# Optimization experiments

Measured on AMD Instinct MI355X. Metric: run time of the kernel, lower is better.

The kernel has to match this reference:

```python
import jax, jax.numpy as jnp
import numpy as np

TEMP = 0.05          # self.temp
NUM_LABELED = 15080  # SysuDataset bank size


def setup_inputs() -> dict:
    key = jax.random.key(0)
    k1, k2, k3, k4, k5 = jax.random.split(key, 5)
    B, D, L = 512, 2048, NUM_LABELED
    f = jax.random.normal(k1, (B, D), jnp.float32)
    features = f / jnp.linalg.norm(f, axis=1, keepdims=True)  # L2-normalized embeddings
    fk = jax.random.normal(k2, (B, D), jnp.float32)
    features_k = fk / jnp.linalg.norm(fk, axis=1, keepdims=True)
    gt_labels = jax.random.randint(k3, (B, 5), 0, L)   # last column = pid index
    gt_labels_k = jax.random.randint(k4, (B, 5), 0, L)
    bank = jax.random.normal(k5, (L, D), jnp.float32)
    bank_features = bank / jnp.linalg.norm(bank, axis=1, keepdims=True)
    return {"features": features, "features_k": features_k,
            "gt_labels": gt_labels, "gt_labels_k": gt_labels_k,
            "bank_features": bank_features}


def reference(features, features_k, gt_labels, gt_labels_k, bank_features):
    # pids = cat([i[:, -1] for i in gt_labels]); all >= 0 by construction, so the
    # pids > -1 filter is an identity (static shapes under jit).
    pids = gt_labels[:, -1]                                  # [B]
    # HM.forward: inputs.mm(features.t()), then /= temp
    sim_all = (features @ bank_features.T) / TEMP            # [B, L]
    # segment-mean of logits grouped by memory label (labels == arange -> identity,
    # kept for faithfulness to the index_add / nums normalization in the source)
    labels = jnp.arange(NUM_LABELED)
    sim = jax.ops.segment_sum(sim_all.T, labels, num_segments=NUM_LABELED)  # [L, B]
    nums = jax.ops.segment_sum(jnp.ones((NUM_LABELED, 1), jnp.float32),
                               labels, num_segments=NUM_LABELED)            # [L, 1]
    sim = sim / nums
    logits = sim.T                                           # [B, L]
    logp = jax.nn.log_softmax(logits, axis=-1)
    loss = -jnp.mean(jnp.take_along_axis(logp, pids[:, None], axis=1))
    return loss
```

## Files before the change

kernel.cpp:

```cpp
#include <hip/hip_runtime.h>
#include <hip/hip_bf16.h>

#define M_ROWS 512
#define N_COLS 15080
#define K_DIM  2048
#define BM 128
#define BN 128
#define BKF 64
#define NT 118
#define KSTEPS (K_DIM / BKF)
#define SCALE 20.0f

typedef _Float16 f16x8 __attribute__((ext_vector_type(8)));
typedef float    f32x4 __attribute__((ext_vector_type(4)));

extern "C" __global__ __launch_bounds__(256, 2)
void k_gemm_lse(const float* __restrict__ A,
                const float* __restrict__ Bk,
                const int*   __restrict__ gt,
                float* __restrict__ pm,
                float* __restrict__ ps,
                float* __restrict__ tv)
{
    __shared__ __align__(16) ushort lds[16384];

    const int t  = threadIdx.x;
    const int bx = blockIdx.x;

    int mi, nt;
    if (bx < 448) {
        const int slot = bx & 7;
        const int rest = bx >> 3;
        mi = rest & 3;
        nt = (rest >> 2) * 8 + slot;
    } else {
        const int r2 = bx - 448;
        mi = r2 & 3;
        nt = 112 + (r2 >> 2);
    }
    const int rowA0 = mi * BM;
    const int rowB0 = nt * BN;

    int arow[4], ag[4];
#pragma unroll
    for (int i = 0; i < 4; i++) { int G = t + i * 256; arow[i] = G >> 3; ag[i] = G & 7; }

    float4 ra[8], rb[8];
    auto LOAD = [&](int kt) {
#pragma unroll
        for (int i = 0; i < 4; i++) {
            const float* pa = A + (size_t)(rowA0 + arow[i]) * K_DIM + kt * BKF + ag[i] * 8;
            ra[2 * i]     = *(const float4*)(pa);
            ra[2 * i + 1] = *(const float4*)(pa + 4);
            const int br = rowB0 + arow[i];
            if (br < N_COLS) {
                const float* pb = Bk + (size_t)br * K_DIM + kt * BKF + ag[i] * 8;
                rb[2 * i]     = *(const float4*)(pb);
                rb[2 * i + 1] = *(const float4*)(pb + 4);
            } else {
                rb[2 * i]     = make_float4(0.f, 0.f, 0.f, 0.f);
                rb[2 * i + 1] = make_float4(0.f, 0.f, 0.f, 0.f);
            }
        }
    };
    auto STORE = [&]() {
#pragma unroll
        for (int i = 0; i < 4; i++) {
            const int ba = (arow[i] * 128 + ag[i] * 16) ^ ((arow[i] & 7) << 4);
            f16x8 ha, hb;
            float4 x = ra[2 * i], y = ra[2 * i + 1];
            ha[0] = (_Float16)x.x; ha[1] = (_Float16)x.y; ha[2] = (_Float16)x.z; ha[3] = (_Float16)x.w;
            ha[4] = (_Float16)y.x; ha[5] = (_Float16)y.y; ha[6] = (_Float16)y.z; ha[7] = (_Float16)y.w;
            x = rb[2 * i]; y = rb[2 * i + 1];
            hb[0] = (_Float16)x.x; hb[1] = (_Float16)x.y; hb[2] = (_Float16)x.z; hb[3] = (_Float16)x.w;
            hb[4] = (_Float16)y.x; hb[5] = (_Float16)y.y; hb[6] = (_Float16)y.z; hb[7] = (_Float16)y.w;
            *(f16x8*)((char*)lds + ba)         = ha;
            *(f16x8*)((char*)lds + 16384 + ba) = hb;
        }
    };

    const int lane = t & 63;
    const int wid  = t >> 6;
    const int wm = wid >> 1, wn = wid & 1;
    const int q = lane >> 4, r = lane & 15;
    int aaddr[4][2], baddr[4][2];
#pragma unroll
    for (int m = 0; m < 4; m++) {
        const int rowa = wm * 64 + m * 16 + r;
        const int rowb = wn * 64 + m * 16 + r;
#pragma unroll
        for (int ks = 0; ks < 2; ks++) {
            aaddr[m][ks] = (rowa * 128 + ks * 64 + q * 16) ^ ((rowa & 7) << 4);
            baddr[m][ks] = 16384 + ((rowb * 128 + ks * 64 + q * 16) ^ ((rowb & 7) << 4));
        }
    }

    f32x4 acc[4][4];
    const f32x4 zero = {0.f, 0.f, 0.f, 0.f};
#pragma unroll
    for (int m = 0; m < 4; m++)
#pragma unroll
        for (int n = 0; n < 4; n++) acc[m][n] = zero;

    LOAD(0);
    for (int kt = 0; kt < KSTEPS; kt++) {
        __syncthreads();
        STORE();
        __syncthreads();
        if (kt + 1 < KSTEPS) LOAD(kt + 1);

        f16x8 bf[4][2];
#pragma unroll
        for (int n = 0; n < 4; n++)
#pragma unroll
            for (int ks = 0; ks < 2; ks++)
                bf[n][ks] = *(const f16x8*)((const char*)lds + baddr[n][ks]);
#pragma unroll
        for (int m = 0; m < 4; m++) {
            const f16x8 af0 = *(const f16x8*)((const char*)lds + aaddr[m][0]);
            const f16x8 af1 = *(const f16x8*)((const char*)lds + aaddr[m][1]);
#pragma unroll
            for (int n = 0; n < 4; n++) {
                acc[m][n] = __builtin_amdgcn_mfma_f32_16x16x32_f16(af0, bf[n][0], acc[m][n], 0, 0, 0);
                acc[m][n] = __builtin_amdgcn_mfma_f32_16x16x32_f16(af1, bf[n][1], acc[m][n], 0, 0, 0);
            }
        }
    }

    __syncthreads();
    float* redm = (float*)lds;
    float* reds = ((float*)lds) + 256;

#pragma unroll
    for (int m = 0; m < 4; m++) {
#pragma unroll
        for (int j = 0; j < 4; j++) {
            const int lrow = wm * 64 + m * 16 + q * 4 + j;
            const int grow = rowA0 + lrow;
            const int pid  = gt[grow * 5 + 4];
            float sv[4];
            float mx = -INFINITY;
#pragma unroll
            for (int n = 0; n < 4; n++) {
                const int gc = rowB0 + wn * 64 + n * 16 + r;
                float s = SCALE * acc[m][n][j];
                s = (gc < N_COLS) ? s : -INFINITY;
                sv[n] = s;
                mx = fmaxf(mx, s);
                if (gc == pid) tv[grow] = s;
            }
#pragma unroll
            for (int d = 1; d < 16; d <<= 1) mx = fmaxf(mx, __shfl_xor(mx, d, 16));
            float se = 0.f;
#pragma unroll
            for (int n = 0; n < 4; n++) se += __expf(sv[n] - mx);
#pragma unroll
            for (int d = 1; d < 16; d <<= 1) se += __shfl_xor(se, d, 16);
            if (r == 0) { redm[wn * 128 + lrow] = mx; reds[wn * 128 + lrow] = se; }
        }
    }
    __syncthreads();
    if (t < 128) {
        const float m0 = redm[t], m1 = redm[128 + t];
        const float s0 = reds[t], s1 = reds[128 + t];
        const float Mv = fmaxf(m0, m1);
        const float Sv = s0 * __expf(m0 - Mv) + s1 * __expf(m1 - Mv);
        pm[nt * 512 + rowA0 + t] = Mv;
        ps[nt * 512 + rowA0 + t] = Sv;
    }
}

extern "C" __global__ void k_reduce(const float* __restrict__ pm,
                                    const float* __restrict__ ps,
                                    const float* __restrict__ tv,
                                    float* __restrict__ out)
{
    __shared__ float red[512];
    const int b = threadIdx.x;
    float M = -INFINITY;
    for (int i = 0; i < NT; i++) M = fmaxf(M, pm[i * 512 + b]);
    float S = 0.f;
    for (int i = 0; i < NT; i++) S += ps[i * 512 + b] * __expf(pm[i * 512 + b] - M);
    const float lb = M + logf(S) - tv[b];
    red[b] = lb;
    __syncthreads();
    for (int s = 256; s > 0; s >>= 1) {
        if (b < s) red[b] += red[b + s];
        __syncthreads();
    }
    if (b == 0) out[0] = red[0] / 512.0f;
}

extern "C" void kernel_launch(void* const* d_in, const int* in_sizes, int n_in,
                              void* d_out, int out_size, void* d_ws, size_t ws_size,
                              hipStream_t stream)
{
    const float* feat = (const float*)d_in[0];
    const int*   gt   = (const int*)d_in[2];
    const float* bank = (const float*)d_in[4];

    float* pm = (float*)d_ws;
    float* ps = pm + NT * 512;
    float* tv = ps + NT * 512;

    k_gemm_lse<<<dim3(4 * NT), 256, 0, stream>>>(feat, bank, gt, pm, ps, tv);
    k_reduce<<<1, 512, 0, stream>>>(pm, ps, tv, (float*)d_out);
}
```

Measured before the change: 285.3 us.

## Use 8-wave GEMM blocks and parallelize the final log-sum-exp reduction

```diff
diff --git a/kernel.cpp b/kernel.cpp
--- a/kernel.cpp
+++ b/kernel.cpp
@@ -14,7 +14,7 @@
 typedef _Float16 f16x8 __attribute__((ext_vector_type(8)));
 typedef float    f32x4 __attribute__((ext_vector_type(4)));
 
-extern "C" __global__ __launch_bounds__(256, 2)
+extern "C" __global__ __launch_bounds__(512, 4)
 void k_gemm_lse(const float* __restrict__ A,
                 const float* __restrict__ Bk,
                 const int*   __restrict__ gt,
@@ -41,14 +41,14 @@
     const int rowA0 = mi * BM;
     const int rowB0 = nt * BN;
 
-    int arow[4], ag[4];
-#pragma unroll
-    for (int i = 0; i < 4; i++) { int G = t + i * 256; arow[i] = G >> 3; ag[i] = G & 7; }
-
-    float4 ra[8], rb[8];
+    int arow[2], ag[2];
+#pragma unroll
+    for (int i = 0; i < 2; i++) { int G = t + i * 512; arow[i] = G >> 3; ag[i] = G & 7; }
+
+    float4 ra[4], rb[4];
     auto LOAD = [&](int kt) {
 #pragma unroll
-        for (int i = 0; i < 4; i++) {
+        for (int i = 0; i < 2; i++) {
             const float* pa = A + (size_t)(rowA0 + arow[i]) * K_DIM + kt * BKF + ag[i] * 8;
             ra[2 * i]     = *(const float4*)(pa);
             ra[2 * i + 1] = *(const float4*)(pa + 4);
@@ -65,7 +65,7 @@
     };
     auto STORE = [&]() {
 #pragma unroll
-        for (int i = 0; i < 4; i++) {
+        for (int i = 0; i < 2; i++) {
             const int ba = (arow[i] * 128 + ag[i] * 16) ^ ((arow[i] & 7) << 4);
             f16x8 ha, hb;
             float4 x = ra[2 * i], y = ra[2 * i + 1];
@@ -81,26 +81,30 @@
 
     const int lane = t & 63;
     const int wid  = t >> 6;
-    const int wm = wid >> 1, wn = wid & 1;
+    const int wm = wid >> 2, wn = wid & 3;
     const int q = lane >> 4, r = lane & 15;
-    int aaddr[4][2], baddr[4][2];
+    int aaddr[4][2], baddr[2][2];
 #pragma unroll
     for (int m = 0; m < 4; m++) {
         const int rowa = wm * 64 + m * 16 + r;
-        const int rowb = wn * 64 + m * 16 + r;
-#pragma unroll
-        for (int ks = 0; ks < 2; ks++) {
+#pragma unroll
+        for (int ks = 0; ks < 2; ks++)
             aaddr[m][ks] = (rowa * 128 + ks * 64 + q * 16) ^ ((rowa & 7) << 4);
-            baddr[m][ks] = 16384 + ((rowb * 128 + ks * 64 + q * 16) ^ ((rowb & 7) << 4));
-        }
-    }
-
-    f32x4 acc[4][4];
+    }
+#pragma unroll
+    for (int n = 0; n < 2; n++) {
+        const int rowb = wn * 32 + n * 16 + r;
+#pragma unroll
+        for (int ks = 0; ks < 2; ks++)
+            baddr[n][ks] = 16384 + ((rowb * 128 + ks * 64 + q * 16) ^ ((rowb & 7) << 4));
+    }
+
+    f32x4 acc[4][2];
     const f32x4 zero = {0.f, 0.f, 0.f, 0.f};
 #pragma unroll
     for (int m = 0; m < 4; m++)
 #pragma unroll
-        for (int n = 0; n < 4; n++) acc[m][n] = zero;
+        for (int n = 0; n < 2; n++) acc[m][n] = zero;
 
     LOAD(0);
     for (int kt = 0; kt < KSTEPS; kt++) {
@@ -109,9 +113,9 @@
         __syncthreads();
         if (kt + 1 < KSTEPS) LOAD(kt + 1);
 
-        f16x8 bf[4][2];
-#pragma unroll
-        for (int n = 0; n < 4; n++)
+        f16x8 bf[2][2];
+#pragma unroll
+        for (int n = 0; n < 2; n++)
 #pragma unroll
             for (int ks = 0; ks < 2; ks++)
                 bf[n][ks] = *(const f16x8*)((const char*)lds + baddr[n][ks]);
@@ -120,7 +124,7 @@
             const f16x8 af0 = *(const f16x8*)((const char*)lds + aaddr[m][0]);
             const f16x8 af1 = *(const f16x8*)((const char*)lds + aaddr[m][1]);
 #pragma unroll
-            for (int n = 0; n < 4; n++) {
+            for (int n = 0; n < 2; n++) {
                 acc[m][n] = __builtin_amdgcn_mfma_f32_16x16x32_f16(af0, bf[n][0], acc[m][n], 0, 0, 0);
                 acc[m][n] = __builtin_amdgcn_mfma_f32_16x16x32_f16(af1, bf[n][1], acc[m][n], 0, 0, 0);
             }
@@ -129,7 +133,7 @@
 
     __syncthreads();
     float* redm = (float*)lds;
-    float* reds = ((float*)lds) + 256;
+    float* reds = ((float*)lds) + 512;
 
 #pragma unroll
     for (int m = 0; m < 4; m++) {
@@ -138,11 +142,11 @@
             const int lrow = wm * 64 + m * 16 + q * 4 + j;
             const int grow = rowA0 + lrow;
             const int pid  = gt[grow * 5 + 4];
-            float sv[4];
+            float sv[2];
             float mx = -INFINITY;
 #pragma unroll
-            for (int n = 0; n < 4; n++) {
-                const int gc = rowB0 + wn * 64 + n * 16 + r;
+            for (int n = 0; n < 2; n++) {
+                const int gc = rowB0 + wn * 32 + n * 16 + r;
                 float s = SCALE * acc[m][n][j];
                 s = (gc < N_COLS) ? s : -INFINITY;
                 sv[n] = s;
@@ -153,7 +157,7 @@
             for (int d = 1; d < 16; d <<= 1) mx = fmaxf(mx, __shfl_xor(mx, d, 16));
             float se = 0.f;
 #pragma unroll
-            for (int n = 0; n < 4; n++) se += __expf(sv[n] - mx);
+            for (int n = 0; n < 2; n++) se += __expf(sv[n] - mx);
 #pragma unroll
             for (int d = 1; d < 16; d <<= 1) se += __shfl_xor(se, d, 16);
             if (r == 0) { redm[wn * 128 + lrow] = mx; reds[wn * 128 + lrow] = se; }
@@ -161,28 +165,55 @@
     }
     __syncthreads();
     if (t < 128) {
-        const float m0 = redm[t], m1 = redm[128 + t];
-        const float s0 = reds[t], s1 = reds[128 + t];
-        const float Mv = fmaxf(m0, m1);
-        const float Sv = s0 * __expf(m0 - Mv) + s1 * __expf(m1 - Mv);
-        pm[nt * 512 + rowA0 + t] = Mv;
-        ps[nt * 512 + rowA0 + t] = Sv;
-    }
-}
-
-extern "C" __global__ void k_reduce(const float* __restrict__ pm,
-                                    const float* __restrict__ ps,
-                                    const float* __restrict__ tv,
-                                    float* __restrict__ out)
+        float Mv = -INFINITY;
+#pragma unroll
+        for (int c = 0; c < 4; c++) Mv = fmaxf(Mv, redm[c * 128 + t]);
+        float Sv = 0.f;
+#pragma unroll
+        for (int c = 0; c < 4; c++) Sv += reds[c * 128 + t] * __expf(redm[c * 128 + t] - Mv);
+        pm[(rowA0 + t) * NT + nt] = Mv;
+        ps[(rowA0 + t) * NT + nt] = Sv;
+    }
+}
+
+extern "C" __global__ __launch_bounds__(128)
+void k_rowlse(const float* __restrict__ pm,
+              const float* __restrict__ ps,
+              const float* __restrict__ tv,
+              float* __restrict__ rowloss)
+{
+    const int b = blockIdx.x;
+    const int i = threadIdx.x;
+    __shared__ float wred[4];
+
+    const float m = (i < NT) ? pm[b * NT + i] : -INFINITY;
+    const float s = (i < NT) ? ps[b * NT + i] : 0.f;
+
+    float M = m;
+#pragma unroll
+    for (int d = 1; d < 64; d <<= 1) M = fmaxf(M, __shfl_xor(M, d, 64));
+    if ((i & 63) == 0) wred[i >> 6] = M;
+    __syncthreads();
+    M = fmaxf(wred[0], wred[1]);
+    __syncthreads();
+
+    float e = (i < NT) ? s * __expf(m - M) : 0.f;
+#pragma unroll
+    for (int d = 1; d < 64; d <<= 1) e += __shfl_xor(e, d, 64);
+    if ((i & 63) == 0) wred[i >> 6] = e;
+    __syncthreads();
+    if (i == 0) {
+        const float S = wred[0] + wred[1];
+        rowloss[b] = M + logf(S) - tv[b];
+    }
+}
+
+extern "C" __global__ __launch_bounds__(512)
+void k_final(const float* __restrict__ rowloss, float* __restrict__ out)
 {
     __shared__ float red[512];
     const int b = threadIdx.x;
-    float M = -INFINITY;
-    for (int i = 0; i < NT; i++) M = fmaxf(M, pm[i * 512 + b]);
-    float S = 0.f;
-    for (int i = 0; i < NT; i++) S += ps[i * 512 + b] * __expf(pm[i * 512 + b] - M);
-    const float lb = M + logf(S) - tv[b];
-    red[b] = lb;
+    red[b] = rowloss[b];
     __syncthreads();
     for (int s = 256; s > 0; s >>= 1) {
         if (b < s) red[b] += red[b + s];
@@ -200,9 +231,11 @@
     const float* bank = (const float*)d_in[4];
 
     float* pm = (float*)d_ws;
-    float* ps = pm + NT * 512;
-    float* tv = ps + NT * 512;
-
-    k_gemm_lse<<<dim3(4 * NT), 256, 0, stream>>>(feat, bank, gt, pm, ps, tv);
-    k_reduce<<<1, 512, 0, stream>>>(pm, ps, tv, (float*)d_out);
-}
+    float* ps = pm + 512 * NT;
+    float* tv = ps + 512 * NT;
+    float* rl = tv + 512;
+
+    k_gemm_lse<<<dim3(4 * NT), 512, 0, stream>>>(feat, bank, gt, pm, ps, tv);
+    k_rowlse<<<dim3(512), 128, 0, stream>>>(pm, ps, tv, rl);
+    k_final<<<dim3(1), 512, 0, stream>>>(rl, (float*)d_out);
+}
```

Result: faster. 250.1 us (-12.3%).
